# Performance work log

Hardware: AMD Instinct MI355X
Metric: run time of the kernel (lower is better)

The kernel has to match this reference:

```python
import jax, jax.numpy as jnp
import numpy as np
import math

FANO_LINES = [(0,1,2),(0,3,4),(0,6,5),(1,3,5),(1,4,6),(2,3,6),(2,5,4)]
WINDOW = 16

def fano_mask(T: int) -> jnp.ndarray:
    """[7,T,T] bool mask: head h attends to j if (j%7 in line_h and j<=i) or i-WINDOW<=j<=i."""
    membership = np.zeros((7, 7), dtype=bool)
    for h, line in enumerate(FANO_LINES):
        membership[h, list(line)] = True
    j = np.arange(T)
    fano = membership[:, j % 7]                      # [7,T]
    i = j[:, None]
    causal = (j[None, :] <= i)                       # [T,T]
    local = causal & (j[None, :] >= i - WINDOW)      # [T,T]
    mask = (fano[:, None, :] & causal[None]) | local[None]
    return jnp.asarray(mask)

def setup_inputs() -> dict:
    key = jax.random.key(0)
    ks = jax.random.split(key, 5)
    B, T, D = 1, 4096, 896
    s = 1.0 / math.sqrt(D)
    return {
        "x":  jax.random.normal(ks[0], (B, T, D), dtype=jnp.float32),
        "Wq": jax.random.normal(ks[1], (D, D), dtype=jnp.float32) * s,
        "Wk": jax.random.normal(ks[2], (D, D), dtype=jnp.float32) * s,
        "Wv": jax.random.normal(ks[3], (D, D), dtype=jnp.float32) * s,
        "Wo": jax.random.normal(ks[4], (D, D), dtype=jnp.float32) * s,
    }

def reference(x, Wq, Wk, Wv, Wo):
    B, T, D = x.shape
    H = 7
    hd = D // H
    # torch Linear: x @ W.T
    q = (x @ Wq.T).reshape(B, T, H, hd)
    k = (x @ Wk.T).reshape(B, T, H, hd)
    v = (x @ Wv.T).reshape(B, T, H, hd)
    scale = 1.0 / math.sqrt(hd)
    scores = jnp.einsum('bthc,bshc->bhts', q, k) * scale   # [B,7,T,T]
    mask = fano_mask(T)                                    # [7,T,T]
    neg = jnp.asarray(-jnp.inf, dtype=scores.dtype)
    scores = jnp.where(mask[None], scores, neg)
    attn = jax.nn.softmax(scores, axis=-1)
    out = jnp.einsum('bhts,bshc->bthc', attn, v).reshape(B, T, D)
    return out @ Wo.T
```

## Files before the change

### kernel.cpp

```cpp
#include <hip/hip_runtime.h>
#include <stdint.h>

typedef unsigned short ushort_t;
typedef __bf16 bf16x8 __attribute__((ext_vector_type(8)));
typedef __bf16 bf16x2 __attribute__((ext_vector_type(2)));
typedef float f32x4 __attribute__((ext_vector_type(4)));

#define T_SEQ 4096
#define D_MODEL 896
#define CHUNKS_PER_BLOCK 4
#define MAXSPLIT 8

#define LSK 136
#define LSV 72

__constant__ int d_LINEMASK[7] = {0x07, 0x19, 0x61, 0x2A, 0x52, 0x4C, 0x34};
__constant__ int d_R[7][3] = {{0,1,2},{0,3,4},{0,5,6},{1,3,5},{1,4,6},{2,3,6},{2,4,5}};

__device__ inline unsigned f2bf(float f) {
    unsigned x = __float_as_uint(f);
    return (x + 0x7fffu + ((x >> 16) & 1u)) >> 16;
}
__device__ inline float lo_f(unsigned x) { return __uint_as_float(x << 16); }
__device__ inline float hi_f(unsigned x) { return __uint_as_float(x & 0xFFFF0000u); }

__device__ __forceinline__ unsigned pk_bf2(float lo, float hi) {
    union { bf16x2 h; unsigned u; } cv;
    cv.h = (bf16x2){(__bf16)lo, (__bf16)hi};
    return cv.u;
}
__device__ __forceinline__ ushort_t bf1(float f) {
    union { __bf16 h; ushort_t u; } cv;
    cv.h = (__bf16)f;
    return cv.u;
}

__host__ __device__ inline int nsplit_of(int t) {
    int a = (192 * t + 189) / 7 + 3;
    int nch_ub = (a + 63) >> 6;
    return (nch_ub + 2 + CHUNKS_PER_BLOCK - 1) / CHUNKS_PER_BLOCK;
}

__global__ __launch_bounds__(256)
void cvt5(const float* __restrict__ x,  const float* __restrict__ wq,
          const float* __restrict__ wk, const float* __restrict__ wv,
          const float* __restrict__ wo,
          ushort_t* __restrict__ xb,  ushort_t* __restrict__ wqb,
          ushort_t* __restrict__ wkb, ushort_t* __restrict__ wvb,
          ushort_t* __restrict__ wob) {
    const int ten = blockIdx.y;
    const float* s = (ten == 0) ? x : (ten == 1) ? wq : (ten == 2) ? wk
                   : (ten == 3) ? wv : wo;
    ushort_t* d = (ten == 0) ? xb : (ten == 1) ? wqb : (ten == 2) ? wkb
                : (ten == 3) ? wvb : wob;
    const int n8 = ((ten == 0) ? T_SEQ * D_MODEL : D_MODEL * D_MODEL) >> 3;
    for (int i = blockIdx.x * 256 + threadIdx.x; i < n8; i += gridDim.x * 256) {
        float4 a = ((const float4*)s)[2 * i];
        float4 b = ((const float4*)s)[2 * i + 1];
        uint4 u;
        u.x = f2bf(a.x) | (f2bf(a.y) << 16);
        u.y = f2bf(a.z) | (f2bf(a.w) << 16);
        u.z = f2bf(b.x) | (f2bf(b.y) << 16);
        u.w = f2bf(b.z) | (f2bf(b.w) << 16);
        ((uint4*)d)[i] = u;
    }
}

__device__ __forceinline__ void async_cp16(const void* g, void* l) {
    __builtin_amdgcn_global_load_lds(
        (__attribute__((address_space(1))) void*)g,
        (__attribute__((address_space(3))) void*)l,
        16, 0, 0);
}

template <bool C32>
__global__ __launch_bounds__(256)
void gemm_nt_dma(const ushort_t* __restrict__ A,
                 const ushort_t* __restrict__ B0,
                 const ushort_t* __restrict__ B1,
                 const ushort_t* __restrict__ B2,
                 void* __restrict__ C0,
                 void* __restrict__ C1,
                 void* __restrict__ C2) {
    const int z = blockIdx.z;
    const ushort_t* B = (z == 0) ? B0 : (z == 1) ? B1 : B2;
    void* C = (z == 0) ? C0 : (z == 1) ? C1 : C2;

    const int K = D_MODEL, N = D_MODEL;
    const int i0 = blockIdx.x * 128;
    const int n0 = blockIdx.y * 128;

    __shared__ __align__(16) ushort_t As[128 * 32];
    __shared__ __align__(16) ushort_t Bs[128 * 32];

    const int t = threadIdx.x;
    const int w = t >> 6, lane = t & 63;
    const int wm = (w >> 1) * 64, wn = (w & 1) * 64;
    const int lr = lane & 15, lq = lane >> 4;

    const int srow = w * 16 + (lane >> 2);
    const int scol = (lane & 3) * 8;
    const ushort_t* gA0 = A + (size_t)(i0 + srow) * K + scol;
    const ushort_t* gA1 = A + (size_t)(i0 + 64 + srow) * K + scol;
    const ushort_t* gB0 = B + (size_t)(n0 + srow) * K + scol;
    const ushort_t* gB1 = B + (size_t)(n0 + 64 + srow) * K + scol;
    ushort_t* lA0 = &As[(w * 16) * 32];
    ushort_t* lA1 = &As[(64 + w * 16) * 32];
    ushort_t* lB0 = &Bs[(w * 16) * 32];
    ushort_t* lB1 = &Bs[(64 + w * 16) * 32];

    f32x4 acc[4][4];
#pragma unroll
    for (int a = 0; a < 4; a++)
#pragma unroll
        for (int b = 0; b < 4; b++) acc[a][b] = (f32x4){0.f, 0.f, 0.f, 0.f};

    for (int k0 = 0; k0 < K; k0 += 32) {
        __syncthreads();
        async_cp16(gA0 + k0, lA0);
        async_cp16(gA1 + k0, lA1);
        async_cp16(gB0 + k0, lB0);
        async_cp16(gB1 + k0, lB1);
        __builtin_amdgcn_s_waitcnt(0);
        __syncthreads();

        bf16x8 af[4], bfr[4];
#pragma unroll
        for (int mi = 0; mi < 4; mi++)
            af[mi] = *(const bf16x8*)&As[(wm + mi * 16 + lr) * 32 + lq * 8];
#pragma unroll
        for (int ni = 0; ni < 4; ni++)
            bfr[ni] = *(const bf16x8*)&Bs[(wn + ni * 16 + lr) * 32 + lq * 8];
#pragma unroll
        for (int mi = 0; mi < 4; mi++)
#pragma unroll
            for (int ni = 0; ni < 4; ni++)
                acc[mi][ni] = __builtin_amdgcn_mfma_f32_16x16x32_bf16(
                    af[mi], bfr[ni], acc[mi][ni], 0, 0, 0);
    }

    if (C32) {
        float* Cf = (float*)C;
#pragma unroll
        for (int mi = 0; mi < 4; mi++)
#pragma unroll
            for (int ni = 0; ni < 4; ni++)
#pragma unroll
                for (int r = 0; r < 4; r++) {
                    int row = i0 + wm + mi * 16 + lq * 4 + r;
                    int col = n0 + wn + ni * 16 + lr;
                    Cf[(size_t)row * N + col] = acc[mi][ni][r];
                }
    } else {
        ushort_t* Cb = (ushort_t*)C;
#pragma unroll
        for (int mi = 0; mi < 4; mi++)
#pragma unroll
            for (int ni = 0; ni < 4; ni++)
#pragma unroll
                for (int r = 0; r < 4; r++) {
                    int row = i0 + wm + mi * 16 + lq * 4 + r;
                    int col = n0 + wn + ni * 16 + lr;
                    Cb[(size_t)row * N + col] = (ushort_t)f2bf(acc[mi][ni][r]);
                }
    }
}

__device__ inline void vt_scatter8(ushort_t* vtcol, uint4 vv) {
    vtcol[0 * LSV] = (ushort_t)(vv.x & 0xFFFFu);
    vtcol[1 * LSV] = (ushort_t)(vv.x >> 16);
    vtcol[2 * LSV] = (ushort_t)(vv.y & 0xFFFFu);
    vtcol[3 * LSV] = (ushort_t)(vv.y >> 16);
    vtcol[4 * LSV] = (ushort_t)(vv.z & 0xFFFFu);
    vtcol[5 * LSV] = (ushort_t)(vv.z >> 16);
    vtcol[6 * LSV] = (ushort_t)(vv.w & 0xFFFFu);
    vtcol[7 * LSV] = (ushort_t)(vv.w >> 16);
}

__device__ inline int jof(int p, int r0, int r1, int r2) {
    int g = p / 3, rs = p - 3 * g;
    return 7 * g + ((rs == 0) ? r0 : (rs == 1) ? r1 : r2);
}

__device__ __forceinline__ void issue_kv(const ushort_t* __restrict__ Kb,
                                         const ushort_t* __restrict__ Vb,
                                         int j, int h, int dim0,
                                         uint4 kreg[4], uint4 vreg[4]) {
    if (j >= 0 && j < T_SEQ) {
        const ushort_t* kp = Kb + (size_t)j * D_MODEL + h * 128 + dim0;
        const ushort_t* vp = Vb + (size_t)j * D_MODEL + h * 128 + dim0;
#pragma unroll
        for (int v = 0; v < 4; v++) {
            kreg[v] = *(const uint4*)(kp + v * 8);
            vreg[v] = *(const uint4*)(vp + v * 8);
        }
    } else {
        uint4 zz = {0u, 0u, 0u, 0u};
#pragma unroll
        for (int v = 0; v < 4; v++) { kreg[v] = zz; vreg[v] = zz; }
    }
}

__device__ __forceinline__ void write_kv(ushort_t* Ks, ushort_t* Vt,
                                         int kk, int dim0,
                                         const uint4 kreg[4], const uint4 vreg[4]) {
#pragma unroll
    for (int v = 0; v < 4; v++) {
        *(uint4*)&Ks[kk * LSK + dim0 + v * 8] = kreg[v];
        vt_scatter8(&Vt[(dim0 + v * 8) * LSV + kk], vreg[v]);
    }
}

__global__ __launch_bounds__(256, 3)
void fano_attn_split(const ushort_t* __restrict__ Qb,
                     const ushort_t* __restrict__ Kb,
                     const ushort_t* __restrict__ Vb,
                     ushort_t* __restrict__ Opart,
                     float* __restrict__ Lm) {
    const int h = blockIdx.y;
    const int p = (int)gridDim.x - 1 - (int)blockIdx.x;

    int tile = 63, pbase0 = 0;
    for (int u = 0; u < 64; ++u) {
        int s = nsplit_of(u);
        if (p < pbase0 + s) { tile = u; break; }
        pbase0 += s;
    }
    const int sp = p - pbase0;
    const int Sloc = nsplit_of(tile);

    const int i0 = tile * 64;
    const int t = threadIdx.x;
    const int w = t >> 6, lane = t & 63;
    const int lr = lane & 15, quad = lane >> 4;
    const int iw0 = i0 + w * 16;

    __shared__ __align__(16) ushort_t Ks[64 * LSK];
    __shared__ __align__(16) ushort_t Vt[128 * LSV];

    const int lm = d_LINEMASK[h];
    const int r0 = d_R[h][0], r1 = d_R[h][1], r2 = d_R[h][2];
    const float scale = 0.08838834764831845f;

    bf16x8 qf[4];
    {
        const ushort_t* qrow = Qb + (size_t)(iw0 + lr) * D_MODEL + h * 128;
#pragma unroll
        for (int f = 0; f < 4; f++)
            qf[f] = *(const bf16x8*)(qrow + f * 32 + quad * 8);
    }

    f32x4 O[8];
#pragma unroll
    for (int dt = 0; dt < 8; dt++) O[dt] = (f32x4){0.f, 0.f, 0.f, 0.f};
    float m = -1e30f;
    float l = 0.f;

    const int imax = i0 + 63;
    const int ncomp = (imax - r0) / 7 + (imax - r1) / 7 + (imax - r2) / 7 + 3;
    const int nch = (ncomp + 63) >> 6;
    const int ntot = nch + 2;
    const int cstart = (sp * ntot) / Sloc;
    const int cend = ((sp + 1) * ntot) / Sloc;

    auto chunk_j = [&](int cc) -> int {
        if (cc >= nch) {
            const int jbase = (cc == nch) ? i0 - 16 : i0 + 48;
            return jbase + lane;
        }
        return jof(cc * 64 + lane, r0, r1, r2);
    };

    uint4 kreg[4], vreg[4];
    if (cstart < cend)
        issue_kv(Kb, Vb, chunk_j(cstart), h, w * 32, kreg, vreg);

    const int iq = iw0 + lr;

    for (int cc = cstart; cc < cend; cc++) {
        const bool band = (cc >= nch);
        const int jbase = (cc == nch) ? i0 - 16 : i0 + 48;

        __syncthreads();
        write_kv(Ks, Vt, lane, w * 32, kreg, vreg);
        __syncthreads();

        if (cc + 1 < cend)
            issue_kv(Kb, Vb, chunk_j(cc + 1), h, w * 32, kreg, vreg);

        {
            int jmin = band ? jbase : jof(cc * 64, r0, r1, r2);
            if (jmin > iw0 + 15) continue;
        }

        f32x4 S[4];
#pragma unroll
        for (int tn = 0; tn < 4; tn++) S[tn] = (f32x4){0.f, 0.f, 0.f, 0.f};
#pragma unroll
        for (int f = 0; f < 4; f++) {
            bf16x8 kf[4];
#pragma unroll
            for (int tn = 0; tn < 4; tn++)
                kf[tn] = *(const bf16x8*)&Ks[(tn * 16 + lr) * LSK + f * 32 + quad * 8];
#pragma unroll
            for (int tn = 0; tn < 4; tn++)
                S[tn] = __builtin_amdgcn_mfma_f32_16x16x32_bf16(kf[tn], qf[f], S[tn], 0, 0, 0);
        }

        const bool interior = !band && (jof(cc * 64 + 63, r0, r1, r2) <= iw0);
        if (interior) {
#pragma unroll
            for (int tn = 0; tn < 4; tn++)
#pragma unroll
                for (int r = 0; r < 4; r++) S[tn][r] *= scale;
        } else if (band) {
#pragma unroll
            for (int tn = 0; tn < 4; tn++)
#pragma unroll
                for (int r = 0; r < 4; r++) {
                    int j = jbase + tn * 16 + quad * 4 + r;
                    int jm = ((j % 7) + 7) % 7;
                    bool ok = (j >= 0) && !((lm >> jm) & 1) &&
                              (j <= iq) && (j >= iq - 16);
                    S[tn][r] = ok ? S[tn][r] * scale : -1e30f;
                }
        } else {
#pragma unroll
            for (int tn = 0; tn < 4; tn++) {
                int p0 = cc * 64 + tn * 16 + quad * 4;
                int g = p0 / 3, rs = p0 - 3 * g;
#pragma unroll
                for (int r = 0; r < 4; r++) {
                    int j = 7 * g + ((rs == 0) ? r0 : (rs == 1) ? r1 : r2);
                    S[tn][r] = (j <= iq) ? S[tn][r] * scale : -1e30f;
                    if (++rs == 3) { rs = 0; ++g; }
                }
            }
        }

        float cm = -1e30f;
#pragma unroll
        for (int tn = 0; tn < 4; tn++)
#pragma unroll
            for (int r = 0; r < 4; r++) cm = fmaxf(cm, S[tn][r]);
        cm = fmaxf(cm, __shfl_xor(cm, 16));
        cm = fmaxf(cm, __shfl_xor(cm, 32));

        const bool defer = __all(cm <= m + 8.f && m >= -60.f);
        float mn, a = 1.f;
        if (defer) {
            mn = m;
        } else {
            mn = fmaxf(fmaxf(m, cm), -60.f);
            a = __expf(m - mn);
            m = mn;
        }
        float pr[4][4];
        float rs_ = 0.f;
#pragma unroll
        for (int tn = 0; tn < 4; tn++)
#pragma unroll
            for (int r = 0; r < 4; r++) {
                pr[tn][r] = __expf(S[tn][r] - mn);
                rs_ += pr[tn][r];
            }
        rs_ += __shfl_xor(rs_, 16);
        rs_ += __shfl_xor(rs_, 32);
        if (defer) {
            l = l + rs_;
        } else {
            l = l * a + rs_;
            float a4[4];
#pragma unroll
            for (int r = 0; r < 4; r++) a4[r] = __shfl(a, quad * 4 + r);
#pragma unroll
            for (int dt = 0; dt < 8; dt++)
#pragma unroll
                for (int r = 0; r < 4; r++) O[dt][r] *= a4[r];
        }

        unsigned u01[4], u23[4];
#pragma unroll
        for (int tn = 0; tn < 4; tn++) {
            u01[tn] = pk_bf2(pr[tn][0], pr[tn][1]);
            u23[tn] = pk_bf2(pr[tn][2], pr[tn][3]);
        }
        const int srcA = 32 * (quad & 1) + lr;
        const int srcB = srcA + 16;
        const bool hi = (quad >= 2);
        uint4 t0, t1;
        {
            unsigned d0a = __shfl(u01[0], srcA), d0b = __shfl(u01[1], srcA);
            unsigned d1a = __shfl(u23[0], srcA), d1b = __shfl(u23[1], srcA);
            unsigned d2a = __shfl(u01[0], srcB), d2b = __shfl(u01[1], srcB);
            unsigned d3a = __shfl(u23[0], srcB), d3b = __shfl(u23[1], srcB);
            t0.x = hi ? d0b : d0a;
            t0.y = hi ? d1b : d1a;
            t0.z = hi ? d2b : d2a;
            t0.w = hi ? d3b : d3a;
        }
        {
            unsigned d0a = __shfl(u01[2], srcA), d0b = __shfl(u01[3], srcA);
            unsigned d1a = __shfl(u23[2], srcA), d1b = __shfl(u23[3], srcA);
            unsigned d2a = __shfl(u01[2], srcB), d2b = __shfl(u01[3], srcB);
            unsigned d3a = __shfl(u23[2], srcB), d3b = __shfl(u23[3], srcB);
            t1.x = hi ? d0b : d0a;
            t1.y = hi ? d1b : d1a;
            t1.z = hi ? d2b : d2a;
            t1.w = hi ? d3b : d3a;
        }
        bf16x8 pf0 = *(const bf16x8*)&t0;
        bf16x8 pf1 = *(const bf16x8*)&t1;

#pragma unroll
        for (int dt = 0; dt < 8; dt++) {
            bf16x8 v0 = *(const bf16x8*)&Vt[(dt * 16 + lr) * LSV + quad * 8];
            bf16x8 v1 = *(const bf16x8*)&Vt[(dt * 16 + lr) * LSV + 32 + quad * 8];
            O[dt] = __builtin_amdgcn_mfma_f32_16x16x32_bf16(pf0, v0, O[dt], 0, 0, 0);
            O[dt] = __builtin_amdgcn_mfma_f32_16x16x32_bf16(pf1, v1, O[dt], 0, 0, 0);
        }
    }

    const size_t pbase = ((size_t)p * 7 + h) * 64;
#pragma unroll
    for (int dt = 0; dt < 8; dt++)
#pragma unroll
        for (int r = 0; r < 4; r++) {
            int lrow = w * 16 + quad * 4 + r;
            Opart[(pbase + lrow) * 128 + dt * 16 + lr] = bf1(O[dt][r]);
        }
    if (quad == 0) {
        int lrow = w * 16 + lr;
        Lm[(pbase + lrow) * 2 + 0] = m;
        Lm[(pbase + lrow) * 2 + 1] = l;
    }
}

__global__ __launch_bounds__(256)
void attn_merge(const ushort_t* __restrict__ Opart,
                const float* __restrict__ Lm,
                ushort_t* __restrict__ Ab) {
    const int h = blockIdx.y;
    const int tt = blockIdx.x;
    int pb = 0;
    for (int u = 0; u < tt; ++u) pb += nsplit_of(u);
    const int S = nsplit_of(tt);
    const int lrow = threadIdx.x >> 2;
    const int row = tt * 64 + lrow;
    const int d0 = (threadIdx.x & 3) * 32;

    float ms[MAXSPLIT], ls[MAXSPLIT], M = -1e30f;
#pragma unroll
    for (int s = 0; s < MAXSPLIT; s++) {
        ms[s] = -1e30f;
        ls[s] = 0.f;
        if (s < S) {
            size_t q = (((size_t)(pb + s) * 7 + h) * 64 + lrow) * 2;
            ms[s] = Lm[q];
            ls[s] = Lm[q + 1];
        }
        M = fmaxf(M, ms[s]);
    }
    float L = 0.f, c[MAXSPLIT];
#pragma unroll
    for (int s = 0; s < MAXSPLIT; s++) {
        c[s] = __expf(ms[s] - M);
        L += c[s] * ls[s];
    }
    float acc[32];
#pragma unroll
    for (int k = 0; k < 32; k++) acc[k] = 0.f;
#pragma unroll
    for (int s = 0; s < MAXSPLIT; s++) {
        if (s < S) {
            const float cs = c[s];
            const ushort_t* op =
                Opart + (((size_t)(pb + s) * 7 + h) * 64 + lrow) * 128 + d0;
#pragma unroll
            for (int v = 0; v < 4; v++) {
                uint4 u = *(const uint4*)(op + v * 8);
                acc[v * 8 + 0] += cs * lo_f(u.x);
                acc[v * 8 + 1] += cs * hi_f(u.x);
                acc[v * 8 + 2] += cs * lo_f(u.y);
                acc[v * 8 + 3] += cs * hi_f(u.y);
                acc[v * 8 + 4] += cs * lo_f(u.z);
                acc[v * 8 + 5] += cs * hi_f(u.z);
                acc[v * 8 + 6] += cs * lo_f(u.w);
                acc[v * 8 + 7] += cs * hi_f(u.w);
            }
        }
    }
    float invL = 1.f / L;
    ushort_t* dst = Ab + (size_t)row * D_MODEL + h * 128 + d0;
#pragma unroll
    for (int v = 0; v < 4; v++) {
        uint4 u;
        u.x = f2bf(acc[v * 8 + 0] * invL) | (f2bf(acc[v * 8 + 1] * invL) << 16);
        u.y = f2bf(acc[v * 8 + 2] * invL) | (f2bf(acc[v * 8 + 3] * invL) << 16);
        u.z = f2bf(acc[v * 8 + 4] * invL) | (f2bf(acc[v * 8 + 5] * invL) << 16);
        u.w = f2bf(acc[v * 8 + 6] * invL) | (f2bf(acc[v * 8 + 7] * invL) << 16);
        *(uint4*)(dst + v * 8) = u;
    }
}

extern "C" void kernel_launch(void* const* d_in, const int* in_sizes, int n_in,
                              void* d_out, int out_size, void* d_ws, size_t ws_size,
                              hipStream_t stream) {
    const float* x  = (const float*)d_in[0];
    const float* Wq = (const float*)d_in[1];
    const float* Wk = (const float*)d_in[2];
    const float* Wv = (const float*)d_in[3];
    const float* Wo = (const float*)d_in[4];

    int NP = 0;
    for (int u = 0; u < 64; ++u) NP += nsplit_of(u);

    const size_t n  = (size_t)T_SEQ * D_MODEL;
    const size_t nw = (size_t)D_MODEL * D_MODEL;
    ushort_t* xb  = (ushort_t*)d_ws + 128;
    ushort_t* Wqb = xb + n;
    ushort_t* Wkb = Wqb + nw;
    ushort_t* Wvb = Wkb + nw;
    ushort_t* Wob = Wvb + nw;
    ushort_t* Qb  = Wob + nw;
    ushort_t* Kb  = Qb + n;
    ushort_t* Vb  = Kb + n;
    ushort_t* Ab  = Vb + n;
    ushort_t* Opart = Ab + n;
    float*    Lm  = (float*)(Opart + (size_t)NP * 7 * 64 * 128);

    cvt5<<<dim3(1792, 5), 256, 0, stream>>>(x, Wq, Wk, Wv, Wo,
                                            xb, Wqb, Wkb, Wvb, Wob);
    gemm_nt_dma<false><<<dim3(32, 7, 3), 256, 0, stream>>>(
        xb, Wqb, Wkb, Wvb, Qb, Kb, Vb);
    fano_attn_split<<<dim3(NP, 7), 256, 0, stream>>>(
        Qb, Kb, Vb, Opart, Lm);
    attn_merge<<<dim3(64, 7), 256, 0, stream>>>(Opart, Lm, Ab);
    gemm_nt_dma<true><<<dim3(32, 7, 1), 256, 0, stream>>>(
        Ab, Wob, Wob, Wob, d_out, d_out, d_out);
}
```

Measured before the change: 129.8 us.

## Drop register prefetch of K/V and raise occupancy to four blocks per CU

Removes the software-pipelined register prefetch of the next K/V chunk and instead loads global K/V and writes it straight into LDS inside the synchronized section. This frees the 32 registers per thread that held the prefetched data, and launch bounds go from 3 to 4 blocks per CU so more waves can hide latency. The cost is that global load latency is no longer overlapped with compute within a block and now sits on the critical path between the barriers.

```diff
diff --git a/kernel.cpp b/kernel.cpp
--- a/kernel.cpp
+++ b/kernel.cpp
@@ -182,36 +182,30 @@
     return 7 * g + ((rs == 0) ? r0 : (rs == 1) ? r1 : r2);
 }
 
-__device__ __forceinline__ void issue_kv(const ushort_t* __restrict__ Kb,
+__device__ __forceinline__ void stage_kv(const ushort_t* __restrict__ Kb,
                                          const ushort_t* __restrict__ Vb,
-                                         int j, int h, int dim0,
-                                         uint4 kreg[4], uint4 vreg[4]) {
+                                         ushort_t* Ks, ushort_t* Vt,
+                                         int j, int kk, int dim0, int h) {
     if (j >= 0 && j < T_SEQ) {
         const ushort_t* kp = Kb + (size_t)j * D_MODEL + h * 128 + dim0;
+#pragma unroll
+        for (int v = 0; v < 4; v++)
+            *(uint4*)&Ks[kk * LSK + dim0 + v * 8] = *(const uint4*)(kp + v * 8);
         const ushort_t* vp = Vb + (size_t)j * D_MODEL + h * 128 + dim0;
 #pragma unroll
-        for (int v = 0; v < 4; v++) {
-            kreg[v] = *(const uint4*)(kp + v * 8);
-            vreg[v] = *(const uint4*)(vp + v * 8);
-        }
+        for (int v = 0; v < 4; v++)
+            vt_scatter8(&Vt[(dim0 + v * 8) * LSV + kk], *(const uint4*)(vp + v * 8));
     } else {
         uint4 zz = {0u, 0u, 0u, 0u};
 #pragma unroll
-        for (int v = 0; v < 4; v++) { kreg[v] = zz; vreg[v] = zz; }
-    }
-}
-
-__device__ __forceinline__ void write_kv(ushort_t* Ks, ushort_t* Vt,
-                                         int kk, int dim0,
-                                         const uint4 kreg[4], const uint4 vreg[4]) {
-#pragma unroll
-    for (int v = 0; v < 4; v++) {
-        *(uint4*)&Ks[kk * LSK + dim0 + v * 8] = kreg[v];
-        vt_scatter8(&Vt[(dim0 + v * 8) * LSV + kk], vreg[v]);
-    }
-}
-
-__global__ __launch_bounds__(256, 3)
+        for (int v = 0; v < 4; v++) {
+            *(uint4*)&Ks[kk * LSK + dim0 + v * 8] = zz;
+            vt_scatter8(&Vt[(dim0 + v * 8) * LSV + kk], zz);
+        }
+    }
+}
+
+__global__ __launch_bounds__(256, 4)
 void fano_attn_split(const ushort_t* __restrict__ Qb,
                      const ushort_t* __restrict__ Kb,
                      const ushort_t* __restrict__ Vb,
@@ -271,10 +265,6 @@
         return jof(cc * 64 + lane, r0, r1, r2);
     };
 
-    uint4 kreg[4], vreg[4];
-    if (cstart < cend)
-        issue_kv(Kb, Vb, chunk_j(cstart), h, w * 32, kreg, vreg);
-
     const int iq = iw0 + lr;
 
     for (int cc = cstart; cc < cend; cc++) {
@@ -282,11 +272,8 @@
         const int jbase = (cc == nch) ? i0 - 16 : i0 + 48;
 
         __syncthreads();
-        write_kv(Ks, Vt, lane, w * 32, kreg, vreg);
+        stage_kv(Kb, Vb, Ks, Vt, chunk_j(cc), lane, w * 32, h);
         __syncthreads();
-
-        if (cc + 1 < cend)
-            issue_kv(Kb, Vb, chunk_j(cc + 1), h, w * 32, kreg, vreg);
 
         {
             int jmin = band ? jbase : jof(cc * 64, r0, r1, r2);
```

Measured after the change: 126.8 us. 1.02x faster.
